# Kernel tuning notes

Measured on AMD Instinct MI355X. Metric: run time of the kernel, lower is better.

Reference implementation:

```python
import jax, jax.numpy as jnp
import numpy as np

N, E, G = 50000, 1250000, 256
IN, H, OUT = 64, 64, 2


def _glorot(k, shape):
    fan = shape[0] + shape[1]
    return jax.random.normal(k, shape, jnp.float32) * np.float32(np.sqrt(2.0 / fan))


def setup_inputs() -> dict:
    key = jax.random.key(0)
    ks = jax.random.split(key, 24)
    inp = {
        "x": jax.random.normal(ks[0], (N, IN), jnp.float32),
        "edge_index": jax.random.randint(ks[1], (2, E), 0, N, dtype=jnp.int32),
        "edge_weight": jax.random.uniform(ks[2], (E,), jnp.float32),
        "batch": jnp.sort(jax.random.randint(ks[3], (N,), 0, G, dtype=jnp.int32)),
    }
    # TransformerConv layer 1 (in=IN -> out=H, heads=1, edge_dim=1)
    inp["Wq1"] = _glorot(ks[4], (IN, H)); inp["bq1"] = jnp.zeros((H,), jnp.float32)
    inp["Wk1"] = _glorot(ks[5], (IN, H)); inp["bk1"] = jnp.zeros((H,), jnp.float32)
    inp["Wv1"] = _glorot(ks[6], (IN, H)); inp["bv1"] = jnp.zeros((H,), jnp.float32)
    inp["We1"] = _glorot(ks[7], (1, H))
    inp["Ws1"] = _glorot(ks[8], (IN, H)); inp["bs1"] = jnp.zeros((H,), jnp.float32)
    # TransformerConv layer 2 (H -> H)
    inp["Wq2"] = _glorot(ks[9], (H, H)); inp["bq2"] = jnp.zeros((H,), jnp.float32)
    inp["Wk2"] = _glorot(ks[10], (H, H)); inp["bk2"] = jnp.zeros((H,), jnp.float32)
    inp["Wv2"] = _glorot(ks[11], (H, H)); inp["bv2"] = jnp.zeros((H,), jnp.float32)
    inp["We2"] = _glorot(ks[12], (1, H))
    inp["Ws2"] = _glorot(ks[13], (H, H)); inp["bs2"] = jnp.zeros((H,), jnp.float32)
    # final linear
    inp["Wl"] = _glorot(ks[14], (H, OUT)); inp["bl"] = jnp.zeros((OUT,), jnp.float32)
    return inp


def _tconv(x, src, dst, e_attr, Wq, bq, Wk, bk, Wv, bv, We, Ws, bs, n):
    # PyG TransformerConv, heads=1, concat=True, root_weight=True, beta=False.
    d = Wq.shape[1]
    q = (x @ Wq + bq)[dst]            # [E, d] gather at target nodes
    k = (x @ Wk + bk)[src]            # [E, d] gather at source nodes
    v = (x @ Wv + bv)[src]            # [E, d]
    e = e_attr @ We                   # [E, d] edge embedding (no bias in PyG)
    alpha = jnp.sum(q * (k + e), axis=-1) / jnp.sqrt(jnp.float32(d))  # [E]
    # segment softmax over incoming edges of each target node
    amax = jax.ops.segment_max(alpha, dst, num_segments=n)
    amax = jnp.where(jnp.isfinite(amax), amax, jnp.float32(0.0))
    ex = jnp.exp(alpha - amax[dst])
    denom = jax.ops.segment_sum(ex, dst, num_segments=n)
    w = ex / jnp.maximum(denom[dst], jnp.float32(1e-16))
    out = jax.ops.segment_sum(w[:, None] * (v + e), dst, num_segments=n)  # [n, d]
    return out + x @ Ws + bs          # skip connection (lin_skip)


def reference(x, edge_index, edge_weight, batch,
              Wq1, bq1, Wk1, bk1, Wv1, bv1, We1, Ws1, bs1,
              Wq2, bq2, Wk2, bk2, Wv2, bv2, We2, Ws2, bs2,
              Wl, bl):
    src, dst = edge_index[0], edge_index[1]
    ea = edge_weight[:, None]  # edge_weight.unsqueeze(-1), edge_dim=1
    n = x.shape[0]
    h = jax.nn.relu(_tconv(x, src, dst, ea, Wq1, bq1, Wk1, bk1, Wv1, bv1, We1, Ws1, bs1, n))
    h = jax.nn.relu(_tconv(h, src, dst, ea, Wq2, bq2, Wk2, bk2, Wv2, bv2, We2, Ws2, bs2, n))
    # global_mean_pool over batch ids
    cnt = jax.ops.segment_sum(jnp.ones((n,), jnp.float32), batch, num_segments=G)
    pooled = jax.ops.segment_sum(h, batch, num_segments=G) / jnp.maximum(cnt, 1.0)[:, None]
    return pooled @ Wl + bl
```

## Files before the change

### kernel.cpp

```cpp
#include <hip/hip_runtime.h>
#include <hip/hip_fp16.h>

#define NN 50000
#define NE 1250000
#define NG 256
#define NBKT 782
#define TILE 4096
#define NTB 306

#define QSCALE 0.18033688011112042f
#define EXP2 __builtin_amdgcn_exp2f

__global__ void k_bcount(const int* __restrict__ dst, int* __restrict__ bcnt) {
    __shared__ int cnt[NBKT];
    for (int i = threadIdx.x; i < NBKT; i += 256) cnt[i] = 0;
    __syncthreads();
    int e0 = blockIdx.x * TILE;
    #pragma unroll
    for (int j = 0; j < 16; j++) {
        int e = e0 + j * 256 + threadIdx.x;
        if (e < NE) atomicAdd(&cnt[dst[e] >> 6], 1);
    }
    __syncthreads();
    for (int i = threadIdx.x; i < NBKT; i += 256)
        if (cnt[i]) atomicAdd(&bcnt[i], cnt[i]);
}

__global__ void k_bscan(const int* __restrict__ bcnt, int* __restrict__ bstart,
                        int* __restrict__ gCursor, int* __restrict__ off) {
    __shared__ int s[256];
    int t = threadIdx.x;
    int c[4]; int sum = 0;
    #pragma unroll
    for (int j = 0; j < 4; j++) {
        int b = t * 4 + j;
        c[j] = (b < NBKT) ? bcnt[b] : 0;
        sum += c[j];
    }
    s[t] = sum;
    __syncthreads();
    for (int o = 1; o < 256; o <<= 1) {
        int tmp = (t >= o) ? s[t - o] : 0;
        __syncthreads();
        s[t] += tmp;
        __syncthreads();
    }
    int run = s[t] - sum;
    #pragma unroll
    for (int j = 0; j < 4; j++) {
        int b = t * 4 + j;
        if (b < NBKT) { bstart[b] = run; gCursor[b] = run; }
        run += c[j];
    }
    if (t == 0) off[NN] = NE;
}

__global__ void k_bscatter(const int* __restrict__ src, const int* __restrict__ dst,
                           const float* __restrict__ ew, int* __restrict__ gCursor,
                           int2* __restrict__ bbuf) {
    __shared__ int cnt[NBKT];
    __shared__ int base[NBKT];
    for (int i = threadIdx.x; i < NBKT; i += 256) cnt[i] = 0;
    __syncthreads();
    int e0 = blockIdx.x * TILE;
    int2 rec[16];
    #pragma unroll
    for (int j = 0; j < 16; j++) {
        int e = e0 + j * 256 + threadIdx.x;
        if (e < NE) {
            int d = dst[e];
            int b = d >> 6;
            rec[j] = make_int2(src[e] | ((d & 63) << 16) | (b << 22), __float_as_int(ew[e]));
            atomicAdd(&cnt[b], 1);
        } else rec[j].x = -1;
    }
    __syncthreads();
    for (int i = threadIdx.x; i < NBKT; i += 256)
        base[i] = cnt[i] ? atomicAdd(&gCursor[i], cnt[i]) : 0;
    __syncthreads();
    #pragma unroll
    for (int j = 0; j < 16; j++) {
        if (rec[j].x != -1) {
            int b = ((unsigned)rec[j].x) >> 22;
            int pos = atomicAdd(&base[b], 1);
            bbuf[pos] = rec[j];
        }
    }
}

__global__ void k_bsort(const int* __restrict__ bcnt, const int* __restrict__ bstart,
                        const int2* __restrict__ bbuf,
                        int* __restrict__ off, unsigned* __restrict__ pairP) {
    int b = blockIdx.x;
    int st = bstart[b], ce = bcnt[b];
    __shared__ int2 sbuf[4096];
    __shared__ int h[64];
    __shared__ int cur[64];
    if (threadIdx.x < 64) h[threadIdx.x] = 0;
    __syncthreads();
    bool fits = (ce <= 4096);
    for (int i = threadIdx.x; i < ce; i += 256) {
        int2 r = bbuf[st + i];
        if (fits) sbuf[i] = r;
        atomicAdd(&h[(r.x >> 16) & 63], 1);
    }
    __syncthreads();
    if (threadIdx.x < 64) {
        int v = h[threadIdx.x];
        int inc = v;
        #pragma unroll
        for (int o = 1; o < 64; o <<= 1) {
            int tmp = __shfl_up(inc, o);
            if (threadIdx.x >= o) inc += tmp;
        }
        int exc = st + inc - v;
        cur[threadIdx.x] = exc;
        int n = b * 64 + threadIdx.x;
        if (n < NN) off[n] = exc;
    }
    __syncthreads();
    for (int i = threadIdx.x; i < ce; i += 256) {
        int2 r = fits ? sbuf[i] : bbuf[st + i];
        int pos = atomicAdd(&cur[(r.x >> 16) & 63], 1);
        unsigned hw = (unsigned)__half_as_ushort(__float2half(__int_as_float(r.y)));
        pairP[pos] = (unsigned)(r.x & 0xFFFF) | (hw << 16);
    }
}

__global__ __launch_bounds__(256, 4)
void k_linear(const float* __restrict__ xin, int relu_in,
              const float* __restrict__ Wq, const float* __restrict__ bq,
              const float* __restrict__ Wk, const float* __restrict__ bk,
              const float* __restrict__ Wv, const float* __restrict__ bv,
              const float* __restrict__ Ws, const float* __restrict__ bs,
              float* __restrict__ q, __half* __restrict__ kvh,
              float* __restrict__ agg) {
    int tid = threadIdx.x;
    int mat = tid >> 6, feat = tid & 63;
    const float* W = mat == 0 ? Wq : mat == 1 ? Wk : mat == 2 ? Wv : Ws;
    const float* b = mat == 0 ? bq : mat == 1 ? bk : mat == 2 ? bv : bs;

    float wcol[64];
    #pragma unroll
    for (int kk = 0; kk < 64; kk++) wcol[kk] = W[kk * 64 + feat];
    float bias = b[feat];
    int kvoff = feat + (mat == 2 ? 64 : 0);

    __shared__ float sx[16 * 64];
    const float4* x4 = (const float4*)xin;

    for (int n0 = blockIdx.x * 16; n0 < NN; n0 += gridDim.x * 16) {
        __syncthreads();
        float4 xv = x4[n0 * 16 + tid];
        if (relu_in) {
            xv.x = fmaxf(xv.x, 0.f); xv.y = fmaxf(xv.y, 0.f);
            xv.z = fmaxf(xv.z, 0.f); xv.w = fmaxf(xv.w, 0.f);
        }
        ((float4*)sx)[tid] = xv;
        __syncthreads();
        for (int c = 0; c < 16; c++) {
            const float4* sxc = (const float4*)(sx + c * 64);
            float a0 = bias, a1 = 0.f, a2 = 0.f, a3 = 0.f;
            #pragma unroll
            for (int k4 = 0; k4 < 16; k4 += 4) {
                float4 v0 = sxc[k4 + 0], v1 = sxc[k4 + 1];
                float4 v2 = sxc[k4 + 2], v3 = sxc[k4 + 3];
                a0 = fmaf(v0.x, wcol[4 * k4 + 0], a0);
                a0 = fmaf(v0.y, wcol[4 * k4 + 1], a0);
                a0 = fmaf(v0.z, wcol[4 * k4 + 2], a0);
                a0 = fmaf(v0.w, wcol[4 * k4 + 3], a0);
                a1 = fmaf(v1.x, wcol[4 * k4 + 4], a1);
                a1 = fmaf(v1.y, wcol[4 * k4 + 5], a1);
                a1 = fmaf(v1.z, wcol[4 * k4 + 6], a1);
                a1 = fmaf(v1.w, wcol[4 * k4 + 7], a1);
                a2 = fmaf(v2.x, wcol[4 * k4 + 8], a2);
                a2 = fmaf(v2.y, wcol[4 * k4 + 9], a2);
                a2 = fmaf(v2.z, wcol[4 * k4 + 10], a2);
                a2 = fmaf(v2.w, wcol[4 * k4 + 11], a2);
                a3 = fmaf(v3.x, wcol[4 * k4 + 12], a3);
                a3 = fmaf(v3.y, wcol[4 * k4 + 13], a3);
                a3 = fmaf(v3.z, wcol[4 * k4 + 14], a3);
                a3 = fmaf(v3.w, wcol[4 * k4 + 15], a3);
            }
            float acc = (a0 + a1) + (a2 + a3);
            int nn = n0 + c;
            if (mat == 0)      q[nn * 64 + feat] = acc * QSCALE;
            else if (mat == 3) agg[nn * 64 + feat] = acc;
            else               kvh[nn * 128 + kvoff] = __float2half(acc);
        }
    }
}

__global__ void k_edge(const unsigned* __restrict__ pairP,
                       const int* __restrict__ off,
                       const float* __restrict__ q, const uint4* __restrict__ kv16,
                       const float* __restrict__ We, float* __restrict__ agg) {
    long gid = (long)blockIdx.x * 256 + threadIdx.x;
    int n = (int)(gid >> 6);
    if (n >= NN) return;
    int lane = threadIdx.x & 63;
    int g = lane >> 3, l = lane & 7;

    const float4* qp = (const float4*)(q + n * 64 + l * 8);
    float4 qa = qp[0], qb = qp[1];
    const float4* wp = (const float4*)(We + l * 8);
    float4 wa = wp[0], wb = wp[1];

    int st = off[n], dg = off[n + 1] - st;

    float qwe = qa.x * wa.x + qa.y * wa.y + qa.z * wa.z + qa.w * wa.w
              + qb.x * wb.x + qb.y * wb.y + qb.z * wb.z + qb.w * wb.w;
    qwe += __shfl_xor(qwe, 1); qwe += __shfl_xor(qwe, 2); qwe += __shfl_xor(qwe, 4);

    float den = 0.f, sw = 0.f;
    float acc[8] = {0.f, 0.f, 0.f, 0.f, 0.f, 0.f, 0.f, 0.f};

    auto edge = [&](unsigned pr, uint4 kk, uint4 vv) {
        float w = __half2float(__ushort_as_half((unsigned short)(pr >> 16)));
        float2 k0 = __half22float2(*(const __half2*)&kk.x);
        float2 k1 = __half22float2(*(const __half2*)&kk.y);
        float2 k2 = __half22float2(*(const __half2*)&kk.z);
        float2 k3 = __half22float2(*(const __half2*)&kk.w);
        float t = qa.x * k0.x;
        t = fmaf(qa.y, k0.y, t); t = fmaf(qa.z, k1.x, t); t = fmaf(qa.w, k1.y, t);
        t = fmaf(qb.x, k2.x, t); t = fmaf(qb.y, k2.y, t);
        t = fmaf(qb.z, k3.x, t); t = fmaf(qb.w, k3.y, t);
        t += __shfl_xor(t, 1); t += __shfl_xor(t, 2); t += __shfl_xor(t, 4);
        t = fmaf(w, qwe, t);
        float p = EXP2(t);
        den += p;
        sw = fmaf(p, w, sw);
        float2 v0 = __half22float2(*(const __half2*)&vv.x);
        float2 v1 = __half22float2(*(const __half2*)&vv.y);
        float2 v2 = __half22float2(*(const __half2*)&vv.z);
        float2 v3 = __half22float2(*(const __half2*)&vv.w);
        acc[0] = fmaf(p, v0.x, acc[0]); acc[1] = fmaf(p, v0.y, acc[1]);
        acc[2] = fmaf(p, v1.x, acc[2]); acc[3] = fmaf(p, v1.y, acc[3]);
        acc[4] = fmaf(p, v2.x, acc[4]); acc[5] = fmaf(p, v2.y, acc[5]);
        acc[6] = fmaf(p, v3.x, acc[6]); acc[7] = fmaf(p, v3.y, acc[7]);
    };

    int nfull = dg >> 3;
    if (nfull > 0) {
        unsigned prA = pairP[st + g];
        unsigned prB = (nfull > 1) ? pairP[st + 8 + g] : 0u;
        unsigned rowA = prA & 0xFFFFu;
        uint4 kkA = kv16[rowA * 16 + l];
        uint4 vvA = kv16[rowA * 16 + 8 + l];
        for (int i = 0; i + 1 < nfull; i++) {
            unsigned prC = (i + 2 < nfull) ? pairP[st + (i + 2) * 8 + g] : 0u;
            unsigned rowB = prB & 0xFFFFu;
            uint4 kkB = kv16[rowB * 16 + l];
            uint4 vvB = kv16[rowB * 16 + 8 + l];
            edge(prA, kkA, vvA);
            prA = prB; kkA = kkB; vvA = vvB; prB = prC;
        }
        edge(prA, kkA, vvA);
    }
    int tl = nfull * 8 + g;
    if (tl < dg) {
        unsigned pr = pairP[st + tl];
        unsigned row = pr & 0xFFFFu;
        uint4 kk = kv16[row * 16 + l];
        uint4 vv = kv16[row * 16 + 8 + l];
        edge(pr, kk, vv);
    }

    #pragma unroll
    for (int o = 8; o <= 32; o <<= 1) {
        den += __shfl_xor(den, o);
        sw  += __shfl_xor(sw, o);
        #pragma unroll
        for (int j = 0; j < 8; j++) acc[j] += __shfl_xor(acc[j], o);
    }

    if (g == 0) {
        float inv = 1.f / fmaxf(den, 1e-16f);
        float swi = sw * inv;
        float4* a4 = (float4*)(agg + n * 64 + l * 8);
        float4 a0 = a4[0], a1 = a4[1];
        a0.x = fmaf(acc[0], inv, fmaf(swi, wa.x, a0.x));
        a0.y = fmaf(acc[1], inv, fmaf(swi, wa.y, a0.y));
        a0.z = fmaf(acc[2], inv, fmaf(swi, wa.z, a0.z));
        a0.w = fmaf(acc[3], inv, fmaf(swi, wa.w, a0.w));
        a1.x = fmaf(acc[4], inv, fmaf(swi, wb.x, a1.x));
        a1.y = fmaf(acc[5], inv, fmaf(swi, wb.y, a1.y));
        a1.z = fmaf(acc[6], inv, fmaf(swi, wb.z, a1.z));
        a1.w = fmaf(acc[7], inv, fmaf(swi, wb.w, a1.w));
        a4[0] = a0; a4[1] = a1;
    }
}

__global__ void k_final(const float* __restrict__ h, const int* __restrict__ batch,
                        const float* __restrict__ Wl, const float* __restrict__ bl,
                        float* __restrict__ out) {
    int g = blockIdx.x;
    int tid = threadIdx.x;
    int lo = 0, hi = NN;
    while (lo < hi) { int mid = (lo + hi) >> 1; if (batch[mid] < g) lo = mid + 1; else hi = mid; }
    int s0 = lo;
    hi = NN;
    while (lo < hi) { int mid = (lo + hi) >> 1; if (batch[mid] < g + 1) lo = mid + 1; else hi = mid; }
    int s1 = lo;

    int sub = tid >> 6, lane = tid & 63;
    float a = 0.f;
    for (int n = s0 + sub; n < s1; n += 4) a += fmaxf(h[n * 64 + lane], 0.f);
    __shared__ float sred[4][64];
    sred[sub][lane] = a;
    __syncthreads();
    if (tid < 64) {
        float p = (sred[0][tid] + sred[1][tid] + sred[2][tid] + sred[3][tid])
                  / fmaxf((float)(s1 - s0), 1.f);
        float a0 = p * Wl[tid * 2 + 0];
        float a1 = p * Wl[tid * 2 + 1];
        #pragma unroll
        for (int o = 1; o < 64; o <<= 1) { a0 += __shfl_xor(a0, o); a1 += __shfl_xor(a1, o); }
        if (tid == 0) { out[g * 2 + 0] = a0 + bl[0]; out[g * 2 + 1] = a1 + bl[1]; }
    }
}

extern "C" void kernel_launch(void* const* d_in, const int* in_sizes, int n_in,
                              void* d_out, int out_size, void* d_ws, size_t ws_size,
                              hipStream_t stream) {
    const float* x    = (const float*)d_in[0];
    const int*   ei   = (const int*)d_in[1];
    const float* ew   = (const float*)d_in[2];
    const int*   batch= (const int*)d_in[3];
    const float *Wq1 = (const float*)d_in[4],  *bq1 = (const float*)d_in[5],
                *Wk1 = (const float*)d_in[6],  *bk1 = (const float*)d_in[7],
                *Wv1 = (const float*)d_in[8],  *bv1 = (const float*)d_in[9],
                *We1 = (const float*)d_in[10], *Ws1 = (const float*)d_in[11],
                *bs1 = (const float*)d_in[12],
                *Wq2 = (const float*)d_in[13], *bq2 = (const float*)d_in[14],
                *Wk2 = (const float*)d_in[15], *bk2 = (const float*)d_in[16],
                *Wv2 = (const float*)d_in[17], *bv2 = (const float*)d_in[18],
                *We2 = (const float*)d_in[19], *Ws2 = (const float*)d_in[20],
                *bs2 = (const float*)d_in[21],
                *Wl  = (const float*)d_in[22], *bl  = (const float*)d_in[23];
    const int* src = ei;
    const int* dst = ei + NE;
    float* out = (float*)d_out;

    float* p = (float*)d_ws;
    float* q    = p; p += (size_t)NN * 64;
    float* agg1 = p; p += (size_t)NN * 64;
    float* agg2 = p; p += (size_t)NN * 64;
    __half* kvh = (__half*)p; p += (size_t)NN * 64;
    int2* bbuf  = (int2*)p;  p += (size_t)NE * 2;
    unsigned* pairP = (unsigned*)p; p += (size_t)NE;
    int* ip = (int*)p;
    int* bcnt    = ip; ip += NBKT;
    int* bstart  = ip; ip += NBKT;
    int* gCursor = ip; ip += NBKT;
    int* off     = ip; ip += NN + 1;

    dim3 b256(256);
    int wgrid = (int)(((long)NN * 64 + 255) / 256);

    hipMemsetAsync(bcnt, 0, NBKT * sizeof(int), stream);
    k_bcount<<<NTB, b256, 0, stream>>>(dst, bcnt);
    k_bscan<<<1, b256, 0, stream>>>(bcnt, bstart, gCursor, off);
    k_bscatter<<<NTB, b256, 0, stream>>>(src, dst, ew, gCursor, bbuf);
    k_bsort<<<NBKT, b256, 0, stream>>>(bcnt, bstart, bbuf, off, pairP);

    k_linear<<<1024, b256, 0, stream>>>(x, 0, Wq1, bq1, Wk1, bk1, Wv1, bv1, Ws1, bs1,
                                        q, kvh, agg1);
    k_edge<<<wgrid, b256, 0, stream>>>(pairP, off, q, (const uint4*)kvh, We1, agg1);

    k_linear<<<1024, b256, 0, stream>>>(agg1, 1, Wq2, bq2, Wk2, bk2, Wv2, bv2, Ws2, bs2,
                                        q, kvh, agg2);
    k_edge<<<wgrid, b256, 0, stream>>>(pairP, off, q, (const uint4*)kvh, We2, agg2);

    k_final<<<NG, b256, 0, stream>>>(agg2, batch, Wl, bl, out);
}
```

Baseline: 237.8 us.

## Vectorize edge bucketing, quantize weights, use fp16 dot2 and fuse ReLU/pool into edge kernel

Several changes land together. The bucketing kernels now load edges as int4 vectors and pack each record into 32 bits, with the edge weight quantized to 10 bits, which halves scatter traffic. The linear kernel drops shared-memory staging and reads rows directly; q is stored in fp16 and the edge kernel uses fdot2 for the attention dots. ReLU is applied inside the edge kernel, and the second layer atomically accumulates the mean pool so a tiny head kernel finishes the job. The 10-bit weight quantization changes numerics, and the pooling atomics may contend per graph.

```diff
diff --git a/kernel.cpp b/kernel.cpp
--- a/kernel.cpp
+++ b/kernel.cpp
@@ -3,6 +3,7 @@
 
 #define NN 50000
 #define NE 1250000
+#define NE4 312500
 #define NG 256
 #define NBKT 782
 #define TILE 4096
@@ -11,15 +12,44 @@
 #define QSCALE 0.18033688011112042f
 #define EXP2 __builtin_amdgcn_exp2f
 
+#if defined(__has_builtin)
+#  if __has_builtin(__builtin_amdgcn_fdot2)
+#    define HAS_FDOT2 1
+#  endif
+#endif
+
+typedef _Float16 h2vec __attribute__((ext_vector_type(2)));
+
+static __device__ __forceinline__ float fdot2f(unsigned a, unsigned b, float c) {
+#ifdef HAS_FDOT2
+    union U { unsigned u; h2vec h; };
+    U ua, ub; ua.u = a; ub.u = b;
+    return __builtin_amdgcn_fdot2(ua.h, ub.h, c, false);
+#else
+    float2 fa = __half22float2(*(const __half2*)&a);
+    float2 fb = __half22float2(*(const __half2*)&b);
+    return fmaf(fa.x, fb.x, fmaf(fa.y, fb.y, c));
+#endif
+}
+
+static __device__ __forceinline__ unsigned h2u(__half2 h) {
+    union { __half2 h; unsigned u; } c; c.h = h; return c.u;
+}
+
 __global__ void k_bcount(const int* __restrict__ dst, int* __restrict__ bcnt) {
     __shared__ int cnt[NBKT];
     for (int i = threadIdx.x; i < NBKT; i += 256) cnt[i] = 0;
     __syncthreads();
-    int e0 = blockIdx.x * TILE;
-    #pragma unroll
-    for (int j = 0; j < 16; j++) {
-        int e = e0 + j * 256 + threadIdx.x;
-        if (e < NE) atomicAdd(&cnt[dst[e] >> 6], 1);
+    const int4* d4 = (const int4*)dst;
+    int b4 = blockIdx.x * (TILE / 4);
+    #pragma unroll
+    for (int j = 0; j < 4; j++) {
+        int i4 = b4 + j * 256 + threadIdx.x;
+        if (i4 < NE4) {
+            int4 d = d4[i4];
+            atomicAdd(&cnt[d.x >> 6], 1); atomicAdd(&cnt[d.y >> 6], 1);
+            atomicAdd(&cnt[d.z >> 6], 1); atomicAdd(&cnt[d.w >> 6], 1);
+        }
     }
     __syncthreads();
     for (int i = threadIdx.x; i < NBKT; i += 256)
@@ -57,22 +87,32 @@
 
 __global__ void k_bscatter(const int* __restrict__ src, const int* __restrict__ dst,
                            const float* __restrict__ ew, int* __restrict__ gCursor,
-                           int2* __restrict__ bbuf) {
+                           unsigned* __restrict__ bbuf) {
     __shared__ int cnt[NBKT];
     __shared__ int base[NBKT];
     for (int i = threadIdx.x; i < NBKT; i += 256) cnt[i] = 0;
     __syncthreads();
-    int e0 = blockIdx.x * TILE;
-    int2 rec[16];
-    #pragma unroll
-    for (int j = 0; j < 16; j++) {
-        int e = e0 + j * 256 + threadIdx.x;
-        if (e < NE) {
-            int d = dst[e];
-            int b = d >> 6;
-            rec[j] = make_int2(src[e] | ((d & 63) << 16) | (b << 22), __float_as_int(ew[e]));
-            atomicAdd(&cnt[b], 1);
-        } else rec[j].x = -1;
+    const int4* s4 = (const int4*)src;
+    const int4* d4 = (const int4*)dst;
+    const float4* w4 = (const float4*)ew;
+    int b4 = blockIdx.x * (TILE / 4);
+    unsigned rec[16]; int bkt[16];
+    #pragma unroll
+    for (int j = 0; j < 4; j++) {
+        int i4 = b4 + j * 256 + threadIdx.x;
+        if (i4 < NE4) {
+            int4 s = s4[i4]; int4 d = d4[i4]; float4 w = w4[i4];
+            int b0 = d.x >> 6, b1 = d.y >> 6, b2 = d.z >> 6, b3 = d.w >> 6;
+            bkt[4*j+0] = b0; bkt[4*j+1] = b1; bkt[4*j+2] = b2; bkt[4*j+3] = b3;
+            rec[4*j+0] = (unsigned)s.x | ((unsigned)(d.x & 63) << 16) | ((unsigned)(w.x * 1023.f + 0.5f) << 22);
+            rec[4*j+1] = (unsigned)s.y | ((unsigned)(d.y & 63) << 16) | ((unsigned)(w.y * 1023.f + 0.5f) << 22);
+            rec[4*j+2] = (unsigned)s.z | ((unsigned)(d.z & 63) << 16) | ((unsigned)(w.z * 1023.f + 0.5f) << 22);
+            rec[4*j+3] = (unsigned)s.w | ((unsigned)(d.w & 63) << 16) | ((unsigned)(w.w * 1023.f + 0.5f) << 22);
+            atomicAdd(&cnt[b0], 1); atomicAdd(&cnt[b1], 1);
+            atomicAdd(&cnt[b2], 1); atomicAdd(&cnt[b3], 1);
+        } else {
+            bkt[4*j+0] = -1; bkt[4*j+1] = -1; bkt[4*j+2] = -1; bkt[4*j+3] = -1;
+        }
     }
     __syncthreads();
     for (int i = threadIdx.x; i < NBKT; i += 256)
@@ -80,29 +120,28 @@
     __syncthreads();
     #pragma unroll
     for (int j = 0; j < 16; j++) {
-        if (rec[j].x != -1) {
-            int b = ((unsigned)rec[j].x) >> 22;
-            int pos = atomicAdd(&base[b], 1);
+        if (bkt[j] >= 0) {
+            int pos = atomicAdd(&base[bkt[j]], 1);
             bbuf[pos] = rec[j];
         }
     }
 }
 
 __global__ void k_bsort(const int* __restrict__ bcnt, const int* __restrict__ bstart,
-                        const int2* __restrict__ bbuf,
+                        const unsigned* __restrict__ bbuf,
                         int* __restrict__ off, unsigned* __restrict__ pairP) {
     int b = blockIdx.x;
     int st = bstart[b], ce = bcnt[b];
-    __shared__ int2 sbuf[4096];
+    __shared__ unsigned sbuf[4096];
     __shared__ int h[64];
     __shared__ int cur[64];
     if (threadIdx.x < 64) h[threadIdx.x] = 0;
     __syncthreads();
     bool fits = (ce <= 4096);
     for (int i = threadIdx.x; i < ce; i += 256) {
-        int2 r = bbuf[st + i];
+        unsigned r = bbuf[st + i];
         if (fits) sbuf[i] = r;
-        atomicAdd(&h[(r.x >> 16) & 63], 1);
+        atomicAdd(&h[(r >> 16) & 63], 1);
     }
     __syncthreads();
     if (threadIdx.x < 64) {
@@ -120,20 +159,21 @@
     }
     __syncthreads();
     for (int i = threadIdx.x; i < ce; i += 256) {
-        int2 r = fits ? sbuf[i] : bbuf[st + i];
-        int pos = atomicAdd(&cur[(r.x >> 16) & 63], 1);
-        unsigned hw = (unsigned)__half_as_ushort(__float2half(__int_as_float(r.y)));
-        pairP[pos] = (unsigned)(r.x & 0xFFFF) | (hw << 16);
+        unsigned r = fits ? sbuf[i] : bbuf[st + i];
+        int pos = atomicAdd(&cur[(r >> 16) & 63], 1);
+        float w = (float)(r >> 22) * (1.f / 1023.f);
+        unsigned hw = (unsigned)__half_as_ushort(__float2half(w));
+        pairP[pos] = (r & 0xFFFFu) | (hw << 16);
     }
 }
 
 __global__ __launch_bounds__(256, 4)
-void k_linear(const float* __restrict__ xin, int relu_in,
+void k_linear(const float* __restrict__ xin,
               const float* __restrict__ Wq, const float* __restrict__ bq,
               const float* __restrict__ Wk, const float* __restrict__ bk,
               const float* __restrict__ Wv, const float* __restrict__ bv,
               const float* __restrict__ Ws, const float* __restrict__ bs,
-              float* __restrict__ q, __half* __restrict__ kvh,
+              __half* __restrict__ qh, __half* __restrict__ kvh,
               float* __restrict__ agg) {
     int tid = threadIdx.x;
     int mat = tid >> 6, feat = tid & 63;
@@ -142,74 +182,52 @@
 
     float wcol[64];
     #pragma unroll
-    for (int kk = 0; kk < 64; kk++) wcol[kk] = W[kk * 64 + feat];
+    for (int k = 0; k < 64; k++) wcol[k] = W[k * 64 + feat];
     float bias = b[feat];
     int kvoff = feat + (mat == 2 ? 64 : 0);
 
-    __shared__ float sx[16 * 64];
-    const float4* x4 = (const float4*)xin;
-
-    for (int n0 = blockIdx.x * 16; n0 < NN; n0 += gridDim.x * 16) {
-        __syncthreads();
-        float4 xv = x4[n0 * 16 + tid];
-        if (relu_in) {
-            xv.x = fmaxf(xv.x, 0.f); xv.y = fmaxf(xv.y, 0.f);
-            xv.z = fmaxf(xv.z, 0.f); xv.w = fmaxf(xv.w, 0.f);
-        }
-        ((float4*)sx)[tid] = xv;
-        __syncthreads();
-        for (int c = 0; c < 16; c++) {
-            const float4* sxc = (const float4*)(sx + c * 64);
-            float a0 = bias, a1 = 0.f, a2 = 0.f, a3 = 0.f;
-            #pragma unroll
-            for (int k4 = 0; k4 < 16; k4 += 4) {
-                float4 v0 = sxc[k4 + 0], v1 = sxc[k4 + 1];
-                float4 v2 = sxc[k4 + 2], v3 = sxc[k4 + 3];
-                a0 = fmaf(v0.x, wcol[4 * k4 + 0], a0);
-                a0 = fmaf(v0.y, wcol[4 * k4 + 1], a0);
-                a0 = fmaf(v0.z, wcol[4 * k4 + 2], a0);
-                a0 = fmaf(v0.w, wcol[4 * k4 + 3], a0);
-                a1 = fmaf(v1.x, wcol[4 * k4 + 4], a1);
-                a1 = fmaf(v1.y, wcol[4 * k4 + 5], a1);
-                a1 = fmaf(v1.z, wcol[4 * k4 + 6], a1);
-                a1 = fmaf(v1.w, wcol[4 * k4 + 7], a1);
-                a2 = fmaf(v2.x, wcol[4 * k4 + 8], a2);
-                a2 = fmaf(v2.y, wcol[4 * k4 + 9], a2);
-                a2 = fmaf(v2.z, wcol[4 * k4 + 10], a2);
-                a2 = fmaf(v2.w, wcol[4 * k4 + 11], a2);
-                a3 = fmaf(v3.x, wcol[4 * k4 + 12], a3);
-                a3 = fmaf(v3.y, wcol[4 * k4 + 13], a3);
-                a3 = fmaf(v3.z, wcol[4 * k4 + 14], a3);
-                a3 = fmaf(v3.w, wcol[4 * k4 + 15], a3);
-            }
-            float acc = (a0 + a1) + (a2 + a3);
-            int nn = n0 + c;
-            if (mat == 0)      q[nn * 64 + feat] = acc * QSCALE;
-            else if (mat == 3) agg[nn * 64 + feat] = acc;
-            else               kvh[nn * 128 + kvoff] = __float2half(acc);
-        }
-    }
-}
-
-__global__ void k_edge(const unsigned* __restrict__ pairP,
-                       const int* __restrict__ off,
-                       const float* __restrict__ q, const uint4* __restrict__ kv16,
-                       const float* __restrict__ We, float* __restrict__ agg) {
+    #pragma unroll 2
+    for (int n = blockIdx.x; n < NN; n += 1024) {
+        const float* xr = xin + (size_t)n * 64;
+        float a0 = bias, a1 = 0.f, a2 = 0.f, a3 = 0.f;
+        #pragma unroll
+        for (int k = 0; k < 64; k += 4) {
+            a0 = fmaf(xr[k + 0], wcol[k + 0], a0);
+            a1 = fmaf(xr[k + 1], wcol[k + 1], a1);
+            a2 = fmaf(xr[k + 2], wcol[k + 2], a2);
+            a3 = fmaf(xr[k + 3], wcol[k + 3], a3);
+        }
+        float acc = (a0 + a1) + (a2 + a3);
+        if (mat == 0)      qh[n * 64 + feat] = __float2half(acc * QSCALE);
+        else if (mat == 3) agg[n * 64 + feat] = acc;
+        else               kvh[n * 128 + kvoff] = __float2half(acc);
+    }
+}
+
+template<int POOL>
+__global__ void k_edge(const unsigned* __restrict__ pairP, const int* __restrict__ off,
+                       const __half* __restrict__ qh, const uint4* __restrict__ kv16,
+                       const float* __restrict__ We, const float* aggin,
+                       float* outp, const int* __restrict__ batch) {
     long gid = (long)blockIdx.x * 256 + threadIdx.x;
     int n = (int)(gid >> 6);
     if (n >= NN) return;
     int lane = threadIdx.x & 63;
     int g = lane >> 3, l = lane & 7;
 
-    const float4* qp = (const float4*)(q + n * 64 + l * 8);
-    float4 qa = qp[0], qb = qp[1];
+    const uint4* q4 = (const uint4*)qh;
+    uint4 qu = q4[n * 8 + l];
     const float4* wp = (const float4*)(We + l * 8);
     float4 wa = wp[0], wb = wp[1];
+    unsigned we01 = h2u(__floats2half2_rn(wa.x, wa.y));
+    unsigned we23 = h2u(__floats2half2_rn(wa.z, wa.w));
+    unsigned we45 = h2u(__floats2half2_rn(wb.x, wb.y));
+    unsigned we67 = h2u(__floats2half2_rn(wb.z, wb.w));
 
     int st = off[n], dg = off[n + 1] - st;
 
-    float qwe = qa.x * wa.x + qa.y * wa.y + qa.z * wa.z + qa.w * wa.w
-              + qb.x * wb.x + qb.y * wb.y + qb.z * wb.z + qb.w * wb.w;
+    float qwe = fdot2f(qu.x, we01, fdot2f(qu.y, we23,
+                fdot2f(qu.z, we45, fdot2f(qu.w, we67, 0.f))));
     qwe += __shfl_xor(qwe, 1); qwe += __shfl_xor(qwe, 2); qwe += __shfl_xor(qwe, 4);
 
     float den = 0.f, sw = 0.f;
@@ -217,27 +235,18 @@
 
     auto edge = [&](unsigned pr, uint4 kk, uint4 vv) {
         float w = __half2float(__ushort_as_half((unsigned short)(pr >> 16)));
-        float2 k0 = __half22float2(*(const __half2*)&kk.x);
-        float2 k1 = __half22float2(*(const __half2*)&kk.y);
-        float2 k2 = __half22float2(*(const __half2*)&kk.z);
-        float2 k3 = __half22float2(*(const __half2*)&kk.w);
-        float t = qa.x * k0.x;
-        t = fmaf(qa.y, k0.y, t); t = fmaf(qa.z, k1.x, t); t = fmaf(qa.w, k1.y, t);
-        t = fmaf(qb.x, k2.x, t); t = fmaf(qb.y, k2.y, t);
-        t = fmaf(qb.z, k3.x, t); t = fmaf(qb.w, k3.y, t);
+        float tA = fdot2f(qu.x, kk.x, fdot2f(qu.y, kk.y, 0.f));
+        float tB = fdot2f(qu.z, kk.z, fdot2f(qu.w, kk.w, 0.f));
+        float t = tA + tB;
         t += __shfl_xor(t, 1); t += __shfl_xor(t, 2); t += __shfl_xor(t, 4);
         t = fmaf(w, qwe, t);
         float p = EXP2(t);
         den += p;
         sw = fmaf(p, w, sw);
-        float2 v0 = __half22float2(*(const __half2*)&vv.x);
-        float2 v1 = __half22float2(*(const __half2*)&vv.y);
-        float2 v2 = __half22float2(*(const __half2*)&vv.z);
-        float2 v3 = __half22float2(*(const __half2*)&vv.w);
-        acc[0] = fmaf(p, v0.x, acc[0]); acc[1] = fmaf(p, v0.y, acc[1]);
-        acc[2] = fmaf(p, v1.x, acc[2]); acc[3] = fmaf(p, v1.y, acc[3]);
-        acc[4] = fmaf(p, v2.x, acc[4]); acc[5] = fmaf(p, v2.y, acc[5]);
-        acc[6] = fmaf(p, v3.x, acc[6]); acc[7] = fmaf(p, v3.y, acc[7]);
+        const __half* vh = (const __half*)&vv;
+        #pragma unroll
+        for (int j = 0; j < 8; j++)
+            acc[j] = fmaf(p, __half2float(vh[j]), acc[j]);
     };
 
     int nfull = dg >> 3;
@@ -277,47 +286,50 @@
     if (g == 0) {
         float inv = 1.f / fmaxf(den, 1e-16f);
         float swi = sw * inv;
-        float4* a4 = (float4*)(agg + n * 64 + l * 8);
-        float4 a0 = a4[0], a1 = a4[1];
-        a0.x = fmaf(acc[0], inv, fmaf(swi, wa.x, a0.x));
-        a0.y = fmaf(acc[1], inv, fmaf(swi, wa.y, a0.y));
-        a0.z = fmaf(acc[2], inv, fmaf(swi, wa.z, a0.z));
-        a0.w = fmaf(acc[3], inv, fmaf(swi, wa.w, a0.w));
-        a1.x = fmaf(acc[4], inv, fmaf(swi, wb.x, a1.x));
-        a1.y = fmaf(acc[5], inv, fmaf(swi, wb.y, a1.y));
-        a1.z = fmaf(acc[6], inv, fmaf(swi, wb.z, a1.z));
-        a1.w = fmaf(acc[7], inv, fmaf(swi, wb.w, a1.w));
-        a4[0] = a0; a4[1] = a1;
-    }
-}
-
-__global__ void k_final(const float* __restrict__ h, const int* __restrict__ batch,
-                        const float* __restrict__ Wl, const float* __restrict__ bl,
-                        float* __restrict__ out) {
-    int g = blockIdx.x;
-    int tid = threadIdx.x;
+        const float4* ain = (const float4*)(aggin + n * 64 + l * 8);
+        float4 a0 = ain[0], a1 = ain[1];
+        a0.x = fmaxf(fmaf(acc[0], inv, fmaf(swi, wa.x, a0.x)), 0.f);
+        a0.y = fmaxf(fmaf(acc[1], inv, fmaf(swi, wa.y, a0.y)), 0.f);
+        a0.z = fmaxf(fmaf(acc[2], inv, fmaf(swi, wa.z, a0.z)), 0.f);
+        a0.w = fmaxf(fmaf(acc[3], inv, fmaf(swi, wa.w, a0.w)), 0.f);
+        a1.x = fmaxf(fmaf(acc[4], inv, fmaf(swi, wb.x, a1.x)), 0.f);
+        a1.y = fmaxf(fmaf(acc[5], inv, fmaf(swi, wb.y, a1.y)), 0.f);
+        a1.z = fmaxf(fmaf(acc[6], inv, fmaf(swi, wb.z, a1.z)), 0.f);
+        a1.w = fmaxf(fmaf(acc[7], inv, fmaf(swi, wb.w, a1.w)), 0.f);
+        if (POOL) {
+            int gg = batch[n];
+            float* pr = outp + gg * 64 + l * 8;
+            atomicAdd(pr + 0, a0.x); atomicAdd(pr + 1, a0.y);
+            atomicAdd(pr + 2, a0.z); atomicAdd(pr + 3, a0.w);
+            atomicAdd(pr + 4, a1.x); atomicAdd(pr + 5, a1.y);
+            atomicAdd(pr + 6, a1.z); atomicAdd(pr + 7, a1.w);
+        } else {
+            float4* ao = (float4*)(outp + n * 64 + l * 8);
+            ao[0] = a0; ao[1] = a1;
+        }
+    }
+}
+
+__global__ void k_head(const float* __restrict__ pooled, const int* __restrict__ batch,
+                       const float* __restrict__ Wl, const float* __restrict__ bl,
+                       float* __restrict__ out) {
+    int g = threadIdx.x;
+    if (g >= NG) return;
     int lo = 0, hi = NN;
     while (lo < hi) { int mid = (lo + hi) >> 1; if (batch[mid] < g) lo = mid + 1; else hi = mid; }
     int s0 = lo;
     hi = NN;
     while (lo < hi) { int mid = (lo + hi) >> 1; if (batch[mid] < g + 1) lo = mid + 1; else hi = mid; }
-    int s1 = lo;
-
-    int sub = tid >> 6, lane = tid & 63;
-    float a = 0.f;
-    for (int n = s0 + sub; n < s1; n += 4) a += fmaxf(h[n * 64 + lane], 0.f);
-    __shared__ float sred[4][64];
-    sred[sub][lane] = a;
-    __syncthreads();
-    if (tid < 64) {
-        float p = (sred[0][tid] + sred[1][tid] + sred[2][tid] + sred[3][tid])
-                  / fmaxf((float)(s1 - s0), 1.f);
-        float a0 = p * Wl[tid * 2 + 0];
-        float a1 = p * Wl[tid * 2 + 1];
-        #pragma unroll
-        for (int o = 1; o < 64; o <<= 1) { a0 += __shfl_xor(a0, o); a1 += __shfl_xor(a1, o); }
-        if (tid == 0) { out[g * 2 + 0] = a0 + bl[0]; out[g * 2 + 1] = a1 + bl[1]; }
-    }
+    float inv = 1.f / fmaxf((float)(lo - s0), 1.f);
+    float a0 = bl[0], a1 = bl[1];
+    #pragma unroll 4
+    for (int f = 0; f < 64; f++) {
+        float p = pooled[g * 64 + f] * inv;
+        a0 = fmaf(p, Wl[2 * f + 0], a0);
+        a1 = fmaf(p, Wl[2 * f + 1], a1);
+    }
+    out[g * 2 + 0] = a0;
+    out[g * 2 + 1] = a1;
 }
 
 extern "C" void kernel_launch(void* const* d_in, const int* in_sizes, int n_in,
@@ -343,34 +355,37 @@
     float* out = (float*)d_out;
 
     float* p = (float*)d_ws;
-    float* q    = p; p += (size_t)NN * 64;
     float* agg1 = p; p += (size_t)NN * 64;
     float* agg2 = p; p += (size_t)NN * 64;
+    __half* qh  = (__half*)p; p += (size_t)NN * 32;
     __half* kvh = (__half*)p; p += (size_t)NN * 64;
-    int2* bbuf  = (int2*)p;  p += (size_t)NE * 2;
+    unsigned* bbuf  = (unsigned*)p; p += (size_t)NE;
     unsigned* pairP = (unsigned*)p; p += (size_t)NE;
-    int* ip = (int*)p;
-    int* bcnt    = ip; ip += NBKT;
-    int* bstart  = ip; ip += NBKT;
-    int* gCursor = ip; ip += NBKT;
-    int* off     = ip; ip += NN + 1;
+    float* pooled = p; p += NG * 64;
+    int* bcnt    = (int*)p; p += NBKT;
+    int* bstart  = (int*)p; p += NBKT;
+    int* gCursor = (int*)p; p += NBKT;
+    int* off     = (int*)p; p += NN + 1;
 
     dim3 b256(256);
     int wgrid = (int)(((long)NN * 64 + 255) / 256);
 
-    hipMemsetAsync(bcnt, 0, NBKT * sizeof(int), stream);
+    hipMemsetAsync(pooled, 0, (size_t)(NG * 64 + NBKT) * sizeof(float), stream);
+
     k_bcount<<<NTB, b256, 0, stream>>>(dst, bcnt);
     k_bscan<<<1, b256, 0, stream>>>(bcnt, bstart, gCursor, off);
     k_bscatter<<<NTB, b256, 0, stream>>>(src, dst, ew, gCursor, bbuf);
     k_bsort<<<NBKT, b256, 0, stream>>>(bcnt, bstart, bbuf, off, pairP);
 
-    k_linear<<<1024, b256, 0, stream>>>(x, 0, Wq1, bq1, Wk1, bk1, Wv1, bv1, Ws1, bs1,
-                                        q, kvh, agg1);
-    k_edge<<<wgrid, b256, 0, stream>>>(pairP, off, q, (const uint4*)kvh, We1, agg1);
-
-    k_linear<<<1024, b256, 0, stream>>>(agg1, 1, Wq2, bq2, Wk2, bk2, Wv2, bv2, Ws2, bs2,
-                                        q, kvh, agg2);
-    k_edge<<<wgrid, b256, 0, stream>>>(pairP, off, q, (const uint4*)kvh, We2, agg2);
-
-    k_final<<<NG, b256, 0, stream>>>(agg2, batch, Wl, bl, out);
-}
+    k_linear<<<1024, b256, 0, stream>>>(x, Wq1, bq1, Wk1, bk1, Wv1, bv1, Ws1, bs1,
+                                        qh, kvh, agg1);
+    k_edge<0><<<wgrid, b256, 0, stream>>>(pairP, off, qh, (const uint4*)kvh, We1,
+                                          agg1, agg1, batch);
+
+    k_linear<<<1024, b256, 0, stream>>>(agg1, Wq2, bq2, Wk2, bk2, Wv2, bv2, Ws2, bs2,
+                                        qh, kvh, agg2);
+    k_edge<1><<<wgrid, b256, 0, stream>>>(pairP, off, qh, (const uint4*)kvh, We2,
+                                          agg2, pooled, batch);
+
+    k_head<<<1, b256, 0, stream>>>(pooled, batch, Wl, bl, out);
+}
```

Result: slower. 441.0 us (+85.5%).
